# Optimization experiments

Hardware: AMD Instinct MI355X
Metric: run time of the kernel (lower is better)

## Reference

```python
import jax, jax.numpy as jnp
import numpy as np
from jax import lax

B = 8192      # batch (many parallel RL envs)
E = 16        # token_embed_size
IE = 128      # image_embed_size == semi_memory_size == LSTM hidden
H = 128       # text GRU hidden (text_embedding_size)
W_EMB = 32    # word_embedding_size
T = 20        # text length
V = 100       # text vocab (obs_space['text'])
NACT = 7      # action_space.n
EMB = IE + H  # embedding_size = 256


def setup_inputs() -> dict:
    key = jax.random.key(0)
    ks = jax.random.split(key, 32)
    f = lambda k, shape, s=0.1: (jax.random.normal(k, shape, jnp.float32) * s)
    C1 = IE // 2
    return {
        'image': jax.random.randint(ks[0], (B, 7, 7, 3), 0, 2),
        'memory': jax.random.normal(ks[1], (B, 2 * IE), jnp.float32),
        'text': jax.random.randint(ks[2], (B, T), 0, V),
        'obj_emb': f(ks[3], (11, E)),
        'col_emb': f(ks[4], (6, E)),
        'st_emb': f(ks[5], (2, E)),
        'conv1_w': f(ks[6], (C1, 3 * E, 2, 2)), 'conv1_b': jnp.zeros((C1,), jnp.float32),
        'conv2_w': f(ks[7], (C1, C1, 2, 2)), 'conv2_b': jnp.zeros((C1,), jnp.float32),
        'conv3_w': f(ks[8], (IE, C1, 2, 2)), 'conv3_b': jnp.zeros((IE,), jnp.float32),
        'lstm_wih': f(ks[9], (4 * IE, IE)), 'lstm_whh': f(ks[10], (4 * IE, IE)),
        'lstm_bih': jnp.zeros((4 * IE,), jnp.float32), 'lstm_bhh': jnp.zeros((4 * IE,), jnp.float32),
        'word_emb': f(ks[11], (V, W_EMB)),
        'gru_wih': f(ks[12], (3 * H, W_EMB)), 'gru_whh': f(ks[13], (3 * H, H)),
        'gru_bih': jnp.zeros((3 * H,), jnp.float32), 'gru_bhh': jnp.zeros((3 * H,), jnp.float32),
        'actor_w1': f(ks[14], (EMB, EMB)), 'actor_b1': jnp.zeros((EMB,), jnp.float32),
        'actor_w2': f(ks[15], (NACT, EMB)), 'actor_b2': jnp.zeros((NACT,), jnp.float32),
        'critic_w1': f(ks[16], (EMB, EMB)), 'critic_b1': jnp.zeros((EMB,), jnp.float32),
        'critic_w2': f(ks[17], (1, EMB)), 'critic_b2': jnp.zeros((1,), jnp.float32),
    }


def reference(image, memory, text, obj_emb, col_emb, st_emb,
              conv1_w, conv1_b, conv2_w, conv2_b, conv3_w, conv3_b,
              lstm_wih, lstm_whh, lstm_bih, lstm_bhh,
              word_emb, gru_wih, gru_whh, gru_bih, gru_bhh,
              actor_w1, actor_b1, actor_w2, actor_b2,
              critic_w1, critic_b1, critic_w2, critic_b2):
    Hs = lstm_whh.shape[1]
    # embed + concat (color, object, state) on last dim, then NHWC->NCHW
    im = jnp.concatenate([col_emb[image[..., 1]], obj_emb[image[..., 0]], st_emb[image[..., 2]]], axis=3)
    x = jnp.transpose(im, (0, 3, 1, 2))  # [B, 3E, 7, 7]
    dn = ('NCHW', 'OIHW', 'NCHW')
    conv = lambda x, w, b: lax.conv_general_dilated(x, w, (1, 1), 'VALID', dimension_numbers=dn) + b[None, :, None, None]
    x = jax.nn.relu(conv(x, conv1_w, conv1_b))                                 # [B, 64, 6, 6]
    x = lax.reduce_window(x, -jnp.inf, lax.max, (1, 1, 2, 2), (1, 1, 2, 2), 'VALID')  # [B, 64, 3, 3]
    x = jax.nn.relu(conv(x, conv2_w, conv2_b))                                 # [B, 64, 2, 2]
    x = jax.nn.relu(conv(x, conv3_w, conv3_b))                                 # [B, 128, 1, 1]
    x = x.reshape(x.shape[0], -1)
    # LSTMCell (torch gate order i, f, g, o)
    h, c = memory[:, :Hs], memory[:, Hs:]
    gates = x @ lstm_wih.T + lstm_bih + h @ lstm_whh.T + lstm_bhh
    i, f, g, o = jnp.split(gates, 4, axis=1)
    c = jax.nn.sigmoid(f) * c + jax.nn.sigmoid(i) * jnp.tanh(g)
    h = jax.nn.sigmoid(o) * jnp.tanh(c)
    memory_out = jnp.concatenate([h, c], axis=1)
    # text GRU (torch gate order r, z, n); precompute input-side gates
    wemb = word_emb[text]  # [B, T, 32]
    gi_all = jnp.einsum('btd,gd->btg', wemb, gru_wih) + gru_bih  # [B, T, 3H]
    HH = gru_whh.shape[1]
    def step(ht, gi):
        gh = ht @ gru_whh.T + gru_bhh
        r = jax.nn.sigmoid(gi[:, :HH] + gh[:, :HH])
        z = jax.nn.sigmoid(gi[:, HH:2 * HH] + gh[:, HH:2 * HH])
        n = jnp.tanh(gi[:, 2 * HH:] + r * gh[:, 2 * HH:])
        return (1.0 - z) * n + z * ht, None
    h0 = jnp.zeros((wemb.shape[0], HH), wemb.dtype)
    ht, _ = lax.scan(step, h0, jnp.swapaxes(gi_all, 0, 1))
    emb = jnp.concatenate([h, ht], axis=1)  # [B, 256]
    logits = jnp.tanh(emb @ actor_w1.T + actor_b1) @ actor_w2.T + actor_b2
    log_probs = jax.nn.log_softmax(logits, axis=1)  # Categorical logits
    value = (jnp.tanh(emb @ critic_w1.T + critic_b1) @ critic_w2.T + critic_b2)[:, 0]
    return (log_probs, value, memory_out)
```

## Files before the change

kernel.cpp:

```cpp
#include <hip/hip_runtime.h>

#define Bsz   8192
#define Tlen  20
#define OUT_VAL_OFF  57344
#define OUT_MEM_OFF  65536

#define WS_GI     0
#define WS_D1     153600
#define WS_WT     161792
#define WS_WHF    686080
#define WS_WTBH   882688
#define WS_WTBL   1144832
#define WS_LB     1406976
#define WS_C2W    1409024
#define WS_C2B    1474560
#define WS_C3W    1474816
#define WS_C3B    1605888
#define WS_C1B    1606400
#define WS_BH     1606656
#define WS_B1     1608192
#define WS_W2     1610240
#define WS_B2     1618432
#define WS_FLAG   1618464
#define WS_WHB    1618496
#define WS_LWTB   1716800

#define GBLK   512
#define GROWS  16
#define PREP_TASKS 404616

using frag16 = __attribute__((ext_vector_type(8))) short;
using fragf4 = __attribute__((ext_vector_type(4))) float;

__device__ __forceinline__ float bf2f(unsigned short u){
    union { unsigned int i; float f; } v; v.i = ((unsigned int)u) << 16; return v.f;
}
__device__ __forceinline__ unsigned short f2bf(float f){
    union { float f; unsigned int i; } v; v.f = f;
    unsigned int x = v.i;
    return (unsigned short)((x + 0x7fffu + ((x >> 16) & 1u)) >> 16);
}
__device__ __forceinline__ float sigm(float x){ return 1.0f / (1.0f + __expf(-x)); }
__device__ __forceinline__ float tanh_f(float x){ return 1.0f - 2.0f / (__expf(2.0f * x) + 1.0f); }

template<bool BF>
__device__ __forceinline__ float G(const void* p, int i){
    if (BF) return bf2f(((const unsigned short*)p)[i]);
    else    return ((const float*)p)[i];
}

__global__ __launch_bounds__(256) void sniff_kernel(
    const unsigned short* __restrict__ we, int* __restrict__ flag)
{
    __shared__ int cnt;
    if (threadIdx.x == 0) cnt = 0;
    __syncthreads();
    int c = 0;
    for (int i = threadIdx.x; i < 2048; i += 256) {
        int e = (we[i] >> 7) & 0xFF;
        if (e >= 96 && e <= 160) c++;
    }
    atomicAdd(&cnt, c);
    __syncthreads();
    if (threadIdx.x == 0) *flag = (cnt >= 1792) ? 1 : 0;
}

template<bool BF>
__global__ __launch_bounds__(256) void prep_kernel(
    const int* __restrict__ flag,
    const void* word_emb, const void* gru_wih, const void* gru_bih,
    const void* col_emb, const void* obj_emb, const void* st_emb,
    const void* conv1_w, const void* conv1_b,
    const void* conv2_w, const void* conv2_b,
    const void* conv3_w, const void* conv3_b,
    const void* lstm_wih, const void* lstm_whh,
    const void* lstm_bih, const void* lstm_bhh,
    const void* actor_w1, const void* actor_b1,
    const void* actor_w2, const void* actor_b2,
    const void* critic_w1, const void* critic_b1,
    const void* critic_w2, const void* critic_b2,
    const void* gru_whh, const void* gru_bhh,
    float* __restrict__ ws0)
{
    if ((*flag != 0) != BF) return;
    int task = blockIdx.x * 256 + threadIdx.x;
    if (task >= PREP_TASKS) return;
    char* wsb = (char*)ws0;
    if (task < 38400) {
        int v = task / 384, g = task - v * 384;
        float acc = G<BF>(gru_bih, g);
        #pragma unroll
        for (int d = 0; d < 32; d++)
            acc += G<BF>(word_emb, v * 32 + d) * G<BF>(gru_wih, g * 32 + d);
        ((float*)(wsb + WS_GI))[task] = acc;
    } else if (task < 40448) {
        int i2 = task - 38400;
        int o = i2 & 63; int tkk = i2 >> 6;
        int kx = tkk & 1, ky = (tkk >> 1) & 1, t = tkk >> 2;
        int c = t & 1, ob = (t >> 1) & 1, s = (t >> 2) & 1;
        float acc = 0.f;
        #pragma unroll
        for (int i = 0; i < 48; i++) {
            float e;
            if (i < 16)      e = G<BF>(col_emb, c * 16 + i);
            else if (i < 32) e = G<BF>(obj_emb, ob * 16 + (i - 16));
            else             e = G<BF>(st_emb, s * 16 + (i - 32));
            acc += e * G<BF>(conv1_w, ((o * 48 + i) * 2 + ky) * 2 + kx);
        }
        ((float*)(wsb + WS_D1))[tkk * 64 + ((o + tkk) & 63)] = acc;
    } else if (task < 171520) {
        int i3 = task - 40448;
        int u = i3 >> 8, k = i3 & 255;
        float w = (u < 256) ? G<BF>(actor_w1, u * 256 + k)
                            : G<BF>(critic_w1, (u - 256) * 256 + k);
        unsigned short hi = f2bf(w);
        ((unsigned short*)(wsb + WS_WTBH))[i3] = hi;
        ((unsigned short*)(wsb + WS_WTBL))[i3] = f2bf(w - bf2f(hi));
    } else if (task < 172032) {
        int i = task - 171520;
        ((float*)(wsb + WS_LB))[i] = G<BF>(lstm_bih, i) + G<BF>(lstm_bhh, i);
    } else if (task < 188416) {
        int i = task - 172032;
        int o = i & 63, pp = (i >> 6) & 3, ii = i >> 8;
        ((float*)(wsb + WS_C2W))[i] = G<BF>(conv2_w, o * 256 + ii * 4 + pp);
    } else if (task < 188480) {
        int i = task - 188416;
        ((float*)(wsb + WS_C2B))[i] = G<BF>(conv2_b, i);
    } else if (task < 221248) {
        int i = task - 188480;
        int o = i & 127, kk = i >> 7;
        ((float*)(wsb + WS_C3W))[i] = G<BF>(conv3_w, o * 256 + kk);
    } else if (task < 221376) {
        int i = task - 221248;
        ((float*)(wsb + WS_C3B))[i] = G<BF>(conv3_b, i);
    } else if (task < 221440) {
        int i = task - 221376;
        ((float*)(wsb + WS_C1B))[i] = G<BF>(conv1_b, i);
    } else if (task < 221824) {
        int i = task - 221440;
        ((float*)(wsb + WS_BH))[i] = G<BF>(gru_bhh, i);
    } else if (task < 222336) {
        int i = task - 221824;
        ((float*)(wsb + WS_B1))[i] = (i < 256) ? G<BF>(actor_b1, i) : G<BF>(critic_b1, i - 256);
    } else if (task < 224384) {
        int i = task - 222336;
        int u = i >> 8, k = i & 255;
        ((float*)(wsb + WS_W2))[i] = (u < 7) ? G<BF>(actor_w2, u * 256 + k) : G<BF>(critic_w2, k);
    } else if (task < 224392) {
        int i = task - 224384;
        ((float*)(wsb + WS_B2))[i] = (i < 7) ? G<BF>(actor_b2, i) : G<BF>(critic_b2, 0);
    } else if (task < 273544) {
        int i = task - 224392;
        ((unsigned short*)(wsb + WS_WHB))[i] = f2bf(G<BF>(gru_whh, i));
    } else {
        int i = task - 273544;
        int g = i >> 8, k = i & 255;
        float v = (k < 128) ? G<BF>(lstm_wih, g * 128 + k)
                            : G<BF>(lstm_whh, g * 128 + (k - 128));
        ((unsigned short*)(wsb + WS_LWTB))[i] = f2bf(v);
    }
}

__global__ __launch_bounds__(256) void conv_kernel(
    const int* __restrict__ image,
    const float* __restrict__ ws0,
    float* __restrict__ mem_out)
{
    const char* wsb = (const char*)ws0;
    const float* D1g  = (const float*)(wsb + WS_D1);
    const float* c1bF = (const float*)(wsb + WS_C1B);
    const float* c2wT = (const float*)(wsb + WS_C2W);
    const float* c2bF = (const float*)(wsb + WS_C2B);
    const float* c3wT = (const float*)(wsb + WS_C3W);
    const float* c3bF = (const float*)(wsb + WS_C3B);

    __shared__ __align__(16) float sp1[576 * 8];
    __shared__ __align__(16) float sp2[256 * 9];
    __shared__ __align__(16) float sD1[2048];
    __shared__ unsigned char stt[392];

    int tid = threadIdx.x;
    int b0 = blockIdx.x * 8;

    for (int i = tid; i < 2048; i += 256) sD1[i] = D1g[i];
    for (int i = tid; i < 392; i += 256) {
        int s = i / 49, p = i - s * 49;
        int base = ((b0 + s) * 49 + p) * 3;
        stt[i] = (unsigned char)(image[base + 1] | (image[base] << 1) | (image[base + 2] << 2));
    }
    __syncthreads();

    for (int task = tid; task < 4608; task += 256) {
        int s = task & 7;
        int op = task >> 3;
        int o = op / 9, p = op - o * 9;
        int py = p / 3, px = p - py * 3;
        float bo = c1bF[o];
        float mx = 0.f;
        #pragma unroll
        for (int dy = 0; dy < 2; dy++)
        #pragma unroll
        for (int dx = 0; dx < 2; dx++) {
            int y = 2 * py + dy, x = 2 * px + dx;
            float sum = bo;
            #pragma unroll
            for (int ky = 0; ky < 2; ky++)
            #pragma unroll
            for (int kx = 0; kx < 2; kx++) {
                int t = stt[s * 49 + (y + ky) * 7 + (x + kx)];
                int tkk = t * 4 + ky * 2 + kx;
                sum += sD1[tkk * 64 + ((o + tkk) & 63)];
            }
            mx = fmaxf(mx, sum);
        }
        sp1[op * 8 + s] = mx;
    }
    __syncthreads();

    {
        int ot = tid & 63, st4 = tid >> 6;
        int s0 = st4 * 2;
        float b = c2bF[ot];
        float acc[4][2];
        #pragma unroll
        for (int p = 0; p < 4; p++) { acc[p][0] = b; acc[p][1] = b; }
        for (int i = 0; i < 64; i++) {
            float w0 = c2wT[(i * 4 + 0) * 64 + ot];
            float w1 = c2wT[(i * 4 + 1) * 64 + ot];
            float w2 = c2wT[(i * 4 + 2) * 64 + ot];
            float w3 = c2wT[(i * 4 + 3) * 64 + ot];
            #pragma unroll
            for (int ss = 0; ss < 2; ss++) {
                const float* vr = sp1 + i * 72 + s0 + ss;
                float v0 = vr[0],  v1 = vr[8],  v2 = vr[16];
                float v3 = vr[24], v4 = vr[32], v5 = vr[40];
                float v6 = vr[48], v7 = vr[56], v8 = vr[64];
                acc[0][ss] += w0 * v0 + w1 * v1 + w2 * v3 + w3 * v4;
                acc[1][ss] += w0 * v1 + w1 * v2 + w2 * v4 + w3 * v5;
                acc[2][ss] += w0 * v3 + w1 * v4 + w2 * v6 + w3 * v7;
                acc[3][ss] += w0 * v4 + w1 * v5 + w2 * v7 + w3 * v8;
            }
        }
        int key = ot >> 3;
        #pragma unroll
        for (int p = 0; p < 4; p++)
            #pragma unroll
            for (int ss = 0; ss < 2; ss++)
                sp2[(ot * 4 + p) * 9 + ((s0 + ss + key) & 7)] = fmaxf(acc[p][ss], 0.f);
    }
    __syncthreads();

    {
        int ot = tid & 127, st2 = tid >> 7;
        int s0 = st2 * 4;
        float b = c3bF[ot];
        float acc[4] = { b, b, b, b };
        for (int kk = 0; kk < 256; kk++) {
            float w = c3wT[kk * 128 + ot];
            const float* ar = sp2 + kk * 9;
            int sw = (kk >> 5) & 7;
            acc[0] = fmaf(w, ar[(s0 + 0 + sw) & 7], acc[0]);
            acc[1] = fmaf(w, ar[(s0 + 1 + sw) & 7], acc[1]);
            acc[2] = fmaf(w, ar[(s0 + 2 + sw) & 7], acc[2]);
            acc[3] = fmaf(w, ar[(s0 + 3 + sw) & 7], acc[3]);
        }
        #pragma unroll
        for (int ss = 0; ss < 4; ss++)
            mem_out[(b0 + s0 + ss) * 256 + ot] = fmaxf(acc[ss], 0.f);
    }
}

#define GI_LOAD(dst, t) do {                                                  \
    _Pragma("unroll")                                                         \
    for (int rg_ = 0; rg_ < 4; rg_++) {                                       \
        int tok_ = sTok2[(m0 + rg_) * Tlen + (t)];                            \
        const float* gp_ = gi_table + tok_ * 384 + j;                         \
        dst[rg_ * 3 + 0] = gp_[0];                                            \
        dst[rg_ * 3 + 1] = gp_[128];                                          \
        dst[rg_ * 3 + 2] = gp_[256];                                          \
    }                                                                         \
} while (0)

#define GRU_STEP(SRD, SWR, GC, GN, T) do {                                    \
    frag16 Af_[4];                                                            \
    _Pragma("unroll")                                                         \
    for (int kc_ = 0; kc_ < 4; kc_++)                                         \
        Af_[kc_] = *(const frag16*)((SRD) + l16 * 136 + kc_ * 32 + quad * 8); \
    fragf4 aR_ = {0.f,0.f,0.f,0.f}, aZ_ = {0.f,0.f,0.f,0.f};                  \
    fragf4 aN_ = {0.f,0.f,0.f,0.f};                                           \
    _Pragma("unroll")                                                         \
    for (int kc_ = 0; kc_ < 4; kc_++) {                                       \
        aR_ = __builtin_amdgcn_mfma_f32_16x16x32_bf16(Af_[kc_], Bf0[kc_], aR_, 0, 0, 0); \
        aZ_ = __builtin_amdgcn_mfma_f32_16x16x32_bf16(Af_[kc_], Bf1[kc_], aZ_, 0, 0, 0); \
        aN_ = __builtin_amdgcn_mfma_f32_16x16x32_bf16(Af_[kc_], Bf2[kc_], aN_, 0, 0, 0); \
    }                                                                         \
    if ((T) < Tlen - 1) GI_LOAD(GN, (T) + 1);                                 \
    _Pragma("unroll")                                                         \
    for (int reg_ = 0; reg_ < 4; reg_++) {                                    \
        float rg2_ = sigm(GC[reg_*3+0] + aR_[reg_] + bh0);                    \
        float zg_  = sigm(GC[reg_*3+1] + aZ_[reg_] + bh1);                    \
        float ng_  = tanh_f(GC[reg_*3+2] + rg2_ * (aN_[reg_] + bh2));         \
        float hn_  = (1.f - zg_) * ng_ + zg_ * hpv[reg_];                     \
        unsigned short hb_ = f2bf(hn_);                                       \
        hpv[reg_] = bf2f(hb_);                                                \
        (SWR)[(m0 + reg_) * 136 + j] = hb_;                                   \
    }                                                                         \
    __syncthreads();                                                          \
} while (0)

__global__ __launch_bounds__(512, 4) void gru_head_kernel(
    const int* __restrict__ flag,
    const int* __restrict__ text, const void* memory,
    const float* __restrict__ ws0,
    float* __restrict__ mem_out,
    float* __restrict__ out_lp, float* __restrict__ out_val)
{
    const char* wsb = (const char*)ws0;
    const unsigned short* whb2 = (const unsigned short*)(wsb + WS_WHB);
    const unsigned short* lwtb = (const unsigned short*)(wsb + WS_LWTB);
    const unsigned short* wtbh = (const unsigned short*)(wsb + WS_WTBH);
    const unsigned short* wtbl = (const unsigned short*)(wsb + WS_WTBL);
    const float* gi_table = (const float*)(wsb + WS_GI);
    const float* bhF      = (const float*)(wsb + WS_BH);
    const float* b1F      = (const float*)(wsb + WS_B1);
    const float* W2f      = (const float*)(wsb + WS_W2);
    const float* B2f      = (const float*)(wsb + WS_B2);
    const float* lbF      = (const float*)(wsb + WS_LB);

    __shared__ __align__(16) unsigned short sHtA[16 * 136];
    __shared__ __align__(16) unsigned short sHtB[16 * 136];
    __shared__ __align__(16) unsigned short sEh[16 * 264];
    __shared__ __align__(16) unsigned short sEl[16 * 264];
    __shared__ __align__(16) float sHid[512 * 16];
    __shared__ float sScore[128];
    __shared__ int   sTok2[320];

    int tid = threadIdx.x;
    int rbase = blockIdx.x * GROWS;
    int wave = tid >> 6, lane = tid & 63;
    int quad = lane >> 4, l16 = lane & 15;
    int j = wave * 16 + l16;
    int m0 = quad * 4;
    const bool bfin = (*flag != 0);
    const unsigned short* mem16 = (const unsigned short*)memory;
    const float*          memf  = (const float*)memory;

    for (int i = tid; i < 4096; i += 512) {
        int m = i >> 8, k = i & 255;
        float v;
        if (k < 128) v = mem_out[(rbase + m) * 256 + k];
        else v = bfin ? bf2f(mem16[(rbase + m) * 256 + (k - 128)])
                      : memf[(rbase + m) * 256 + (k - 128)];
        sEh[m * 264 + k] = f2bf(v);
    }
    for (int i = tid; i < 16 * 136; i += 512) sHtA[i] = 0;
    if (tid < 320) sTok2[tid] = text[rbase * Tlen + tid];
    __syncthreads();

    {
        frag16 Ax[8];
        #pragma unroll
        for (int kc = 0; kc < 8; kc++)
            Ax[kc] = *(const frag16*)(sEh + l16 * 264 + kc * 32 + quad * 8);
        fragf4 aI = {0.f,0.f,0.f,0.f}, aF = {0.f,0.f,0.f,0.f};
        fragf4 aG = {0.f,0.f,0.f,0.f}, aO = {0.f,0.f,0.f,0.f};
        #pragma unroll
        for (int kc = 0; kc < 8; kc++) {
            int ko = kc * 32 + quad * 8;
            frag16 bI = *(const frag16*)(lwtb + (j)       * 256 + ko);
            frag16 bF = *(const frag16*)(lwtb + (128 + j) * 256 + ko);
            frag16 bG = *(const frag16*)(lwtb + (256 + j) * 256 + ko);
            frag16 bO = *(const frag16*)(lwtb + (384 + j) * 256 + ko);
            aI = __builtin_amdgcn_mfma_f32_16x16x32_bf16(Ax[kc], bI, aI, 0, 0, 0);
            aF = __builtin_amdgcn_mfma_f32_16x16x32_bf16(Ax[kc], bF, aF, 0, 0, 0);
            aG = __builtin_amdgcn_mfma_f32_16x16x32_bf16(Ax[kc], bG, aG, 0, 0, 0);
            aO = __builtin_amdgcn_mfma_f32_16x16x32_bf16(Ax[kc], bO, aO, 0, 0, 0);
        }
        float lbI = lbF[j], lbFg = lbF[128 + j], lbG = lbF[256 + j], lbO = lbF[384 + j];
        __syncthreads();
        #pragma unroll
        for (int reg = 0; reg < 4; reg++) {
            int m = m0 + reg;
            float ig = sigm(aI[reg] + lbI);
            float fg = sigm(aF[reg] + lbFg);
            float gv = tanh_f(aG[reg] + lbG);
            float og = sigm(aO[reg] + lbO);
            float cv = bfin ? bf2f(mem16[(rbase + m) * 256 + 128 + j])
                            : memf[(rbase + m) * 256 + 128 + j];
            float cn = fg * cv + ig * gv;
            float hn = og * tanh_f(cn);
            mem_out[(rbase + m) * 256 + j]       = hn;
            mem_out[(rbase + m) * 256 + 128 + j] = cn;
            unsigned short hh = f2bf(hn);
            sEh[m * 264 + j] = hh;
            sEl[m * 264 + j] = f2bf(hn - bf2f(hh));
        }
    }

    frag16 Bf0[4], Bf1[4], Bf2[4];
    #pragma unroll
    for (int kc = 0; kc < 4; kc++) {
        int ko = kc * 32 + quad * 8;
        Bf0[kc] = *(const frag16*)(whb2 + (j)       * 128 + ko);
        Bf1[kc] = *(const frag16*)(whb2 + (128 + j) * 128 + ko);
        Bf2[kc] = *(const frag16*)(whb2 + (256 + j) * 128 + ko);
    }
    float bh0 = bhF[j], bh1 = bhF[128 + j], bh2 = bhF[256 + j];
    float hpv[4] = { 0.f, 0.f, 0.f, 0.f };
    float ga[12], gb[12];

    GI_LOAD(ga, 0);

    for (int tt = 0; tt < 10; tt++) {
        int t0 = tt * 2;
        GRU_STEP(sHtA, sHtB, ga, gb, t0);
        GRU_STEP(sHtB, sHtA, gb, ga, t0 + 1);
    }

    #pragma unroll
    for (int reg = 0; reg < 4; reg++) {
        int m = m0 + reg;
        sEh[m * 264 + 128 + j] = f2bf(hpv[reg]);
        sEl[m * 264 + 128 + j] = 0;
    }
    __syncthreads();

    {
        fragf4 z4 = {0.f,0.f,0.f,0.f};
        fragf4 acc[4];
        #pragma unroll
        for (int jb = 0; jb < 4; jb++) acc[jb] = z4;
        #pragma unroll
        for (int kc = 0; kc < 8; kc++) {
            int ko = kc * 32 + quad * 8;
            frag16 Eh = *(const frag16*)(sEh + l16 * 264 + ko);
            frag16 El = *(const frag16*)(sEl + l16 * 264 + ko);
            #pragma unroll
            for (int jb = 0; jb < 4; jb++) {
                int u = jb * 128 + wave * 16 + l16;
                frag16 Wh = *(const frag16*)(wtbh + u * 256 + ko);
                frag16 Wl = *(const frag16*)(wtbl + u * 256 + ko);
                acc[jb] = __builtin_amdgcn_mfma_f32_16x16x32_bf16(Eh, Wh, acc[jb], 0, 0, 0);
                acc[jb] = __builtin_amdgcn_mfma_f32_16x16x32_bf16(El, Wh, acc[jb], 0, 0, 0);
                acc[jb] = __builtin_amdgcn_mfma_f32_16x16x32_bf16(Eh, Wl, acc[jb], 0, 0, 0);
            }
        }
        #pragma unroll
        for (int jb = 0; jb < 4; jb++) {
            int u = jb * 128 + wave * 16 + l16;
            float bu = b1F[u];
            #pragma unroll
            for (int reg = 0; reg < 4; reg++) {
                int m = m0 + reg;
                sHid[u * 16 + ((m + l16) & 15)] = tanh_f(acc[jb][reg] + bu);
            }
        }
    }
    __syncthreads();

    {
        int r = tid >> 3, i = tid & 7;
        float acc2 = 0.f;
        if (tid < 128) {
            acc2 = B2f[i];
            const float* wrp = W2f + i * 256;
            int ubase = (i < 7) ? 0 : 256;
            for (int k = 0; k < 256; k++) {
                int u = ubase + k;
                acc2 += wrp[k] * sHid[u * 16 + ((r + (u & 15)) & 15)];
            }
            sScore[tid] = acc2;
        }
        __syncthreads();
        if (tid < 128) {
            const float* sr = sScore + r * 8;
            float mx = sr[0];
            #pragma unroll
            for (int a = 1; a < 7; a++) mx = fmaxf(mx, sr[a]);
            float se = 0.f;
            #pragma unroll
            for (int a = 0; a < 7; a++) se += __expf(sr[a] - mx);
            float lse = mx + __logf(se);
            if (i < 7) out_lp[(rbase + r) * 7 + i] = acc2 - lse;
            else       out_val[rbase + r] = acc2;
        }
    }
}

extern "C" void kernel_launch(void* const* d_in, const int* in_sizes, int n_in,
                              void* d_out, int out_size, void* d_ws, size_t ws_size,
                              hipStream_t stream) {
    const int*  image  = (const int*)d_in[0];
    const void* memory = d_in[1];
    const int*  text   = (const int*)d_in[2];

    char* wsb = (char*)d_ws;
    float* ws0  = (float*)wsb;
    int*   flag = (int*)(wsb + WS_FLAG);

    float* out = (float*)d_out;
    float* out_lp  = out;
    float* out_val = out + OUT_VAL_OFF;
    float* mem_out = out + OUT_MEM_OFF;

    sniff_kernel<<<1, 256, 0, stream>>>((const unsigned short*)d_in[16], flag);

    const int PREP_GRID = (PREP_TASKS + 255) / 256;
    prep_kernel<true><<<PREP_GRID, 256, 0, stream>>>(flag,
        d_in[16], d_in[17], d_in[19], d_in[4], d_in[3], d_in[5],
        d_in[6], d_in[7], d_in[8], d_in[9], d_in[10], d_in[11],
        d_in[12], d_in[13], d_in[14], d_in[15],
        d_in[21], d_in[22], d_in[23], d_in[24],
        d_in[25], d_in[26], d_in[27], d_in[28],
        d_in[18], d_in[20], ws0);
    prep_kernel<false><<<PREP_GRID, 256, 0, stream>>>(flag,
        d_in[16], d_in[17], d_in[19], d_in[4], d_in[3], d_in[5],
        d_in[6], d_in[7], d_in[8], d_in[9], d_in[10], d_in[11],
        d_in[12], d_in[13], d_in[14], d_in[15],
        d_in[21], d_in[22], d_in[23], d_in[24],
        d_in[25], d_in[26], d_in[27], d_in[28],
        d_in[18], d_in[20], ws0);

    conv_kernel<<<Bsz / 8, 256, 0, stream>>>(image, ws0, mem_out);

    gru_head_kernel<<<GBLK, 512, 0, stream>>>(flag, text, memory, ws0,
                                              mem_out, out_lp, out_val);
}
```

Before: 280.9 us.

## Alias shared buffers into one union and process head output in two halves

Shared memory buffers are merged into one aliased region, and the hidden-activation buffer now reuses the space of the embedding and GRU state buffers. The head epilogue writes hidden activations and computes scores in two passes of 8 rows each, which halves sHid. This cuts LDS per block from roughly 58KB to about 27KB, so more blocks can be resident per CU. The El correction MFMA is skipped for the upper K half, since the GRU part of El is zero, and that zero store is removed. The extra barriers and the serialized halves add sync overhead in the epilogue.

```diff
diff --git a/kernel.cpp b/kernel.cpp
--- a/kernel.cpp
+++ b/kernel.cpp
@@ -327,13 +327,15 @@
     const float* B2f      = (const float*)(wsb + WS_B2);
     const float* lbF      = (const float*)(wsb + WS_LB);
 
-    __shared__ __align__(16) unsigned short sHtA[16 * 136];
-    __shared__ __align__(16) unsigned short sHtB[16 * 136];
-    __shared__ __align__(16) unsigned short sEh[16 * 264];
-    __shared__ __align__(16) unsigned short sEl[16 * 264];
-    __shared__ __align__(16) float sHid[512 * 16];
-    __shared__ float sScore[128];
+    __shared__ __align__(16) char sU[25600];
+    __shared__ float sScore[64];
     __shared__ int   sTok2[320];
+
+    unsigned short* sEh  = (unsigned short*)sU;
+    unsigned short* sEl  = (unsigned short*)(sU + 8448);
+    unsigned short* sHtA = (unsigned short*)(sU + 16896);
+    unsigned short* sHtB = (unsigned short*)(sU + 21248);
+    float* sHid = (float*)sU;
 
     int tid = threadIdx.x;
     int rbase = blockIdx.x * GROWS;
@@ -353,7 +355,7 @@
                       : memf[(rbase + m) * 256 + (k - 128)];
         sEh[m * 264 + k] = f2bf(v);
     }
-    for (int i = tid; i < 16 * 136; i += 512) sHtA[i] = 0;
+    for (int i = tid; i < 2176; i += 512) sHtA[i] = 0;
     if (tid < 320) sTok2[tid] = text[rbase * Tlen + tid];
     __syncthreads();
 
@@ -421,58 +423,68 @@
     for (int reg = 0; reg < 4; reg++) {
         int m = m0 + reg;
         sEh[m * 264 + 128 + j] = f2bf(hpv[reg]);
-        sEl[m * 264 + 128 + j] = 0;
-    }
-    __syncthreads();
-
+    }
+    __syncthreads();
+
+    fragf4 acc[4];
     {
         fragf4 z4 = {0.f,0.f,0.f,0.f};
-        fragf4 acc[4];
         #pragma unroll
         for (int jb = 0; jb < 4; jb++) acc[jb] = z4;
         #pragma unroll
         for (int kc = 0; kc < 8; kc++) {
             int ko = kc * 32 + quad * 8;
             frag16 Eh = *(const frag16*)(sEh + l16 * 264 + ko);
-            frag16 El = *(const frag16*)(sEl + l16 * 264 + ko);
             #pragma unroll
             for (int jb = 0; jb < 4; jb++) {
                 int u = jb * 128 + wave * 16 + l16;
                 frag16 Wh = *(const frag16*)(wtbh + u * 256 + ko);
                 frag16 Wl = *(const frag16*)(wtbl + u * 256 + ko);
                 acc[jb] = __builtin_amdgcn_mfma_f32_16x16x32_bf16(Eh, Wh, acc[jb], 0, 0, 0);
-                acc[jb] = __builtin_amdgcn_mfma_f32_16x16x32_bf16(El, Wh, acc[jb], 0, 0, 0);
                 acc[jb] = __builtin_amdgcn_mfma_f32_16x16x32_bf16(Eh, Wl, acc[jb], 0, 0, 0);
             }
-        }
-        #pragma unroll
-        for (int jb = 0; jb < 4; jb++) {
-            int u = jb * 128 + wave * 16 + l16;
-            float bu = b1F[u];
-            #pragma unroll
-            for (int reg = 0; reg < 4; reg++) {
-                int m = m0 + reg;
-                sHid[u * 16 + ((m + l16) & 15)] = tanh_f(acc[jb][reg] + bu);
+            if (kc < 4) {
+                frag16 El = *(const frag16*)(sEl + l16 * 264 + ko);
+                #pragma unroll
+                for (int jb = 0; jb < 4; jb++) {
+                    int u = jb * 128 + wave * 16 + l16;
+                    frag16 Wh = *(const frag16*)(wtbh + u * 256 + ko);
+                    acc[jb] = __builtin_amdgcn_mfma_f32_16x16x32_bf16(El, Wh, acc[jb], 0, 0, 0);
+                }
             }
         }
     }
     __syncthreads();
 
-    {
+    #pragma unroll
+    for (int half = 0; half < 2; half++) {
+        if ((quad >> 1) == half) {
+            #pragma unroll
+            for (int jb = 0; jb < 4; jb++) {
+                int u = jb * 128 + wave * 16 + l16;
+                float bu = b1F[u];
+                #pragma unroll
+                for (int reg = 0; reg < 4; reg++) {
+                    int mm = (m0 & 7) + reg;
+                    sHid[u * 8 + ((mm + (u & 7)) & 7)] = tanh_f(acc[jb][reg] + bu);
+                }
+            }
+        }
+        __syncthreads();
+        float acc2 = 0.f;
         int r = tid >> 3, i = tid & 7;
-        float acc2 = 0.f;
-        if (tid < 128) {
+        if (tid < 64) {
             acc2 = B2f[i];
             const float* wrp = W2f + i * 256;
             int ubase = (i < 7) ? 0 : 256;
             for (int k = 0; k < 256; k++) {
                 int u = ubase + k;
-                acc2 += wrp[k] * sHid[u * 16 + ((r + (u & 15)) & 15)];
+                acc2 += wrp[k] * sHid[u * 8 + ((r + (u & 7)) & 7)];
             }
             sScore[tid] = acc2;
         }
         __syncthreads();
-        if (tid < 128) {
+        if (tid < 64) {
             const float* sr = sScore + r * 8;
             float mx = sr[0];
             #pragma unroll
@@ -481,9 +493,11 @@
             #pragma unroll
             for (int a = 0; a < 7; a++) se += __expf(sr[a] - mx);
             float lse = mx + __logf(se);
-            if (i < 7) out_lp[(rbase + r) * 7 + i] = acc2 - lse;
-            else       out_val[rbase + r] = acc2;
-        }
+            int row = rbase + half * 8 + r;
+            if (i < 7) out_lp[row * 7 + i] = acc2 - lse;
+            else       out_val[row] = acc2;
+        }
+        if (half == 0) __syncthreads();
     }
 }
 
```

Measured after the change: 279.9 us. No clear change (-0.4%).
